# Optimization experiments

Hardware: AMD Instinct MI355X
Metric: run time of the kernel (lower is better)

## Reference

```python
import jax, jax.numpy as jnp
import numpy as np

KAPPA = 5.0
EPS_NORM = 1e-12  # torch F.normalize eps
EPS_LOG = 1e-09


def setup_inputs() -> dict:
    key = jax.random.key(0)
    student_output = jax.random.normal(key, (16384, 256), dtype=jnp.float32)
    return {"student_output": student_output}


def reference(student_output) -> jnp.ndarray:
    # L2-normalize rows (matches F.normalize: x / max(||x||, eps))
    norm = jnp.linalg.norm(student_output, axis=-1, keepdims=True)
    x_norm = student_output / jnp.maximum(norm, EPS_NORM)
    # pairwise cosine similarity [n, n]
    sim = x_norm @ x_norm.T
    kernel = jnp.exp(KAPPA * sim)
    density_estimates = kernel.sum(axis=1)  # [n]
    entropy = -jnp.mean(jnp.log(density_estimates + EPS_LOG))
    return entropy
```

## Files before the change

### kernel.cpp

```cpp
#include <hip/hip_runtime.h>


#define NROWS 16384
#define KDIM 256
#define NTILE 128
#define NT (NROWS / NTILE)
#define NSTRIP 4
#define TOTAL_BLOCKS (NT * NSTRIP)

typedef int i32x4_t __attribute__((ext_vector_type(4)));
typedef int i32x8_t __attribute__((ext_vector_type(8)));
typedef float f32x16_t __attribute__((ext_vector_type(16)));
typedef __attribute__((address_space(1))) const void global_cvoid_t;
typedef __attribute__((address_space(3))) void lds_void_t;

#if __has_builtin(__builtin_amdgcn_exp2f)
#define EXPK(x) __builtin_amdgcn_exp2f((x) * 7.2134752044448f)
#else
#define EXPK(x) __expf(5.0f * (x))
#endif

union frag8 { i32x8_t v8; i32x4_t v4[2]; };

__global__ __launch_bounds__(256)
void kde_normalize(const float* __restrict__ X, unsigned int* __restrict__ Xn8,
                   float* __restrict__ density, unsigned int* __restrict__ ticket) {
  const int wave = threadIdx.x >> 6;
  const int lane = threadIdx.x & 63;
  const int row = blockIdx.x * 4 + wave;
  const float4 v = ((const float4*)(X + (size_t)row * KDIM))[lane];
  float ss = v.x * v.x + v.y * v.y + v.z * v.z + v.w * v.w;
  ss += __shfl_xor(ss, 1);
  ss += __shfl_xor(ss, 2);
  ss += __shfl_xor(ss, 4);
  ss += __shfl_xor(ss, 8);
  ss += __shfl_xor(ss, 16);
  ss += __shfl_xor(ss, 32);
  const float scale = 1.0f / fmaxf(sqrtf(ss), 1e-12f);
  int p = 0;
  p = __builtin_amdgcn_cvt_pk_fp8_f32(v.x * scale, v.y * scale, p, false);
  p = __builtin_amdgcn_cvt_pk_fp8_f32(v.z * scale, v.w * scale, p, true);
  Xn8[(size_t)row * 64 + lane] = (unsigned int)p;
  if (threadIdx.x < 4) density[blockIdx.x * 4 + threadIdx.x] = 0.0f;
  if (blockIdx.x == 0 && threadIdx.x == 0) *ticket = 0u;
}

__global__ __launch_bounds__(256, 2)
void kde_gemm(const unsigned char* __restrict__ Xn8, float* __restrict__ density,
              unsigned int* __restrict__ ticket, float* __restrict__ out) {
  extern __shared__ char smem[];
  char* As = smem;
  char* Bs = smem + 32768;

  const int tid = threadIdx.x;
  const int wave = tid >> 6;
  const int lane = tid & 63;
  const int wr = wave >> 1;
  const int wc = wave & 1;
  const int m32 = lane & 31;
  const int h = lane >> 5;
  const int bi = blockIdx.x;
  const int s = blockIdx.y;
  const int t0 = s * 16;
  const int nt = (s == NSTRIP - 1 && bi < NT / 2) ? 17 : 16;
  const char* Xb = (const char*)Xn8;

#define STAGE(base_row, dst)                                                      \
  for (int c = wave; c < 32; c += 4) {                                            \
    const int rt = c >> 3, kb = (c >> 1) & 3, hh = c & 1;                         \
    const size_t gofs =                                                           \
        (size_t)((base_row) + rt * 32 + m32) * KDIM + kb * 64 + h * 32 + hh * 16; \
    __builtin_amdgcn_global_load_lds((global_cvoid_t*)(Xb + gofs),                \
                                     (lds_void_t*)((dst) + c * 1024), 16, 0, 0);  \
  }

  STAGE(bi * NTILE, As);
  STAGE(((bi + t0) & (NT - 1)) * NTILE, Bs);

  float rs[2][16];
#pragma unroll
  for (int i = 0; i < 2; i++)
#pragma unroll
    for (int r = 0; r < 16; r++) rs[i][r] = 0.0f;

  for (int k = 0; k < nt; ++k) {
    const int t = t0 + k;
    const int J = (bi + t) & (NT - 1);
    __syncthreads();

    f32x16_t acc[2][2];
#pragma unroll
    for (int i = 0; i < 2; i++)
#pragma unroll
      for (int j = 0; j < 2; j++) acc[i][j] = (f32x16_t)0.0f;

#pragma unroll
    for (int kb = 0; kb < 4; ++kb) {
      frag8 af[2], bf[2];
#pragma unroll
      for (int i = 0; i < 2; i++) {
        const char* pa = As + ((wr * 2 + i) * 8 + kb * 2) * 1024 + lane * 16;
        af[i].v4[0] = *(const i32x4_t*)pa;
        af[i].v4[1] = *(const i32x4_t*)(pa + 1024);
        const char* pb = Bs + ((wc * 2 + i) * 8 + kb * 2) * 1024 + lane * 16;
        bf[i].v4[0] = *(const i32x4_t*)pb;
        bf[i].v4[1] = *(const i32x4_t*)(pb + 1024);
      }
#pragma unroll
      for (int i = 0; i < 2; i++)
#pragma unroll
        for (int j = 0; j < 2; j++)
          acc[i][j] = __builtin_amdgcn_mfma_scale_f32_32x32x64_f8f6f4(
              af[i].v8, bf[j].v8, acc[i][j], 0, 0, 0, 127, 0, 127);
    }

    __syncthreads();

    if (k + 1 < nt) STAGE(((J + 1) & (NT - 1)) * NTILE, Bs);

    float cs[2] = {0.0f, 0.0f};
#pragma unroll
    for (int i = 0; i < 2; i++)
#pragma unroll
      for (int j = 0; j < 2; j++)
#pragma unroll
        for (int r = 0; r < 16; r++) {
          const float e = EXPK(acc[i][j][r]);
          rs[i][r] += e;
          cs[j] += e;
        }

    if (t != 0) {
#pragma unroll
      for (int j = 0; j < 2; j++) {
        float v = cs[j] + __shfl_xor(cs[j], 32);
        if (h == 0)
          atomicAdd(&density[J * NTILE + wc * 64 + j * 32 + m32], v);
      }
    }
  }

#pragma unroll
  for (int i = 0; i < 2; i++)
#pragma unroll
    for (int r = 0; r < 16; r++) {
      float v = rs[i][r];
      v += __shfl_xor(v, 1);
      v += __shfl_xor(v, 2);
      v += __shfl_xor(v, 4);
      v += __shfl_xor(v, 8);
      v += __shfl_xor(v, 16);
      if (m32 == 0) {
        const int row = bi * NTILE + wr * 64 + i * 32 + (r & 3) + 8 * (r >> 2) + 4 * h;
        atomicAdd(&density[row], v);
      }
    }
#undef STAGE

  __syncthreads();
  if (tid == 0) {
    __threadfence();
    ((volatile unsigned int*)smem)[0] = atomicAdd(ticket, 1u);
  }
  __syncthreads();
  if (((volatile unsigned int*)smem)[0] == TOTAL_BLOCKS - 1) {
    __threadfence();
    float ssum = 0.0f;
    for (int i = tid; i < NROWS; i += 256) {
      const float d = __hip_atomic_load(&density[i], __ATOMIC_RELAXED,
                                        __HIP_MEMORY_SCOPE_AGENT);
      ssum += logf(d + 1e-9f);
    }
    ssum += __shfl_xor(ssum, 1);
    ssum += __shfl_xor(ssum, 2);
    ssum += __shfl_xor(ssum, 4);
    ssum += __shfl_xor(ssum, 8);
    ssum += __shfl_xor(ssum, 16);
    ssum += __shfl_xor(ssum, 32);
    float* red = ((float*)smem) + 16;
    if (lane == 0) red[wave] = ssum;
    __syncthreads();
    if (tid == 0) out[0] = -(red[0] + red[1] + red[2] + red[3]) / (float)NROWS;
  }
}

extern "C" void kernel_launch(void* const* d_in, const int* in_sizes, int n_in,
                              void* d_out, int out_size, void* d_ws, size_t ws_size,
                              hipStream_t stream) {
  const float* X = (const float*)d_in[0];
  float* out = (float*)d_out;
  char* ws = (char*)d_ws;
  unsigned int* Xn8 = (unsigned int*)ws;
  float* density = (float*)(ws + (size_t)NROWS * KDIM);
  unsigned int* ticket = (unsigned int*)(density + NROWS);

  hipFuncSetAttribute((const void*)kde_gemm,
                      hipFuncAttributeMaxDynamicSharedMemorySize, 65536);

  kde_normalize<<<NROWS / 4, 256, 0, stream>>>(X, Xn8, density, ticket);
  kde_gemm<<<dim3(NT, NSTRIP), 256, 65536, stream>>>((const unsigned char*)ws,
                                                     density, ticket, out);
}
```

Before: 135.2 us.

## Double-buffer B tiles, keep A fragments in registers, fold exp scale into normalization

The B tile now uses two LDS buffers. The next tile is prefetched at the start of each iteration, so the global-to-LDS copy overlaps the MFMA and exp work, and only one barrier remains per iteration. The A tile fragments are loaded from LDS into registers once and reused across all column tiles, which removes repeated LDS reads. The exp scale factor kappa·log2(e) is split as a square root into each normalized row before fp8 quantization, so the exp becomes a bare exp2. The costs are higher register pressure and slightly different fp8 rounding of the scaled values.

```diff
diff --git a/kernel.cpp b/kernel.cpp
--- a/kernel.cpp
+++ b/kernel.cpp
@@ -8,6 +8,8 @@
 #define NSTRIP 4
 #define TOTAL_BLOCKS (NT * NSTRIP)
 
+#define SQRT_KLOG2E 2.68579577857f
+
 typedef int i32x4_t __attribute__((ext_vector_type(4)));
 typedef int i32x8_t __attribute__((ext_vector_type(8)));
 typedef float f32x16_t __attribute__((ext_vector_type(16)));
@@ -15,9 +17,9 @@
 typedef __attribute__((address_space(3))) void lds_void_t;
 
 #if __has_builtin(__builtin_amdgcn_exp2f)
-#define EXPK(x) __builtin_amdgcn_exp2f((x) * 7.2134752044448f)
+#define EXP2(x) __builtin_amdgcn_exp2f(x)
 #else
-#define EXPK(x) __expf(5.0f * (x))
+#define EXP2(x) exp2f(x)
 #endif
 
 union frag8 { i32x8_t v8; i32x4_t v4[2]; };
@@ -36,7 +38,7 @@
   ss += __shfl_xor(ss, 8);
   ss += __shfl_xor(ss, 16);
   ss += __shfl_xor(ss, 32);
-  const float scale = 1.0f / fmaxf(sqrtf(ss), 1e-12f);
+  const float scale = SQRT_KLOG2E / fmaxf(sqrtf(ss), 1e-12f);
   int p = 0;
   p = __builtin_amdgcn_cvt_pk_fp8_f32(v.x * scale, v.y * scale, p, false);
   p = __builtin_amdgcn_cvt_pk_fp8_f32(v.z * scale, v.w * scale, p, true);
@@ -49,8 +51,8 @@
 void kde_gemm(const unsigned char* __restrict__ Xn8, float* __restrict__ density,
               unsigned int* __restrict__ ticket, float* __restrict__ out) {
   extern __shared__ char smem[];
-  char* As = smem;
-  char* Bs = smem + 32768;
+  char* buf0 = smem;
+  char* buf1 = smem + 32768;
 
   const int tid = threadIdx.x;
   const int wave = tid >> 6;
@@ -74,8 +76,20 @@
                                      (lds_void_t*)((dst) + c * 1024), 16, 0, 0);  \
   }
 
-  STAGE(bi * NTILE, As);
-  STAGE(((bi + t0) & (NT - 1)) * NTILE, Bs);
+  STAGE(bi * NTILE, buf0);
+  STAGE(((bi + t0) & (NT - 1)) * NTILE, buf1);
+  __syncthreads();
+
+  frag8 areg[2][4];
+#pragma unroll
+  for (int i = 0; i < 2; i++)
+#pragma unroll
+    for (int kb = 0; kb < 4; kb++) {
+      const char* pa = buf0 + ((wr * 2 + i) * 8 + kb * 2) * 1024 + lane * 16;
+      areg[i][kb].v4[0] = *(const i32x4_t*)pa;
+      areg[i][kb].v4[1] = *(const i32x4_t*)(pa + 1024);
+    }
+  __syncthreads();
 
   float rs[2][16];
 #pragma unroll
@@ -86,7 +100,10 @@
   for (int k = 0; k < nt; ++k) {
     const int t = t0 + k;
     const int J = (bi + t) & (NT - 1);
-    __syncthreads();
+    char* rbuf = (k & 1) ? buf0 : buf1;
+    char* sbuf = (k & 1) ? buf1 : buf0;
+
+    if (k + 1 < nt) STAGE(((J + 1) & (NT - 1)) * NTILE, sbuf);
 
     f32x16_t acc[2][2];
 #pragma unroll
@@ -96,27 +113,20 @@
 
 #pragma unroll
     for (int kb = 0; kb < 4; ++kb) {
-      frag8 af[2], bf[2];
-#pragma unroll
-      for (int i = 0; i < 2; i++) {
-        const char* pa = As + ((wr * 2 + i) * 8 + kb * 2) * 1024 + lane * 16;
-        af[i].v4[0] = *(const i32x4_t*)pa;
-        af[i].v4[1] = *(const i32x4_t*)(pa + 1024);
-        const char* pb = Bs + ((wc * 2 + i) * 8 + kb * 2) * 1024 + lane * 16;
-        bf[i].v4[0] = *(const i32x4_t*)pb;
-        bf[i].v4[1] = *(const i32x4_t*)(pb + 1024);
+      frag8 bf[2];
+#pragma unroll
+      for (int j = 0; j < 2; j++) {
+        const char* pb = rbuf + ((wc * 2 + j) * 8 + kb * 2) * 1024 + lane * 16;
+        bf[j].v4[0] = *(const i32x4_t*)pb;
+        bf[j].v4[1] = *(const i32x4_t*)(pb + 1024);
       }
 #pragma unroll
       for (int i = 0; i < 2; i++)
 #pragma unroll
         for (int j = 0; j < 2; j++)
           acc[i][j] = __builtin_amdgcn_mfma_scale_f32_32x32x64_f8f6f4(
-              af[i].v8, bf[j].v8, acc[i][j], 0, 0, 0, 127, 0, 127);
-    }
-
-    __syncthreads();
-
-    if (k + 1 < nt) STAGE(((J + 1) & (NT - 1)) * NTILE, Bs);
+              areg[i][kb].v8, bf[j].v8, acc[i][j], 0, 0, 0, 127, 0, 127);
+    }
 
     float cs[2] = {0.0f, 0.0f};
 #pragma unroll
@@ -125,7 +135,7 @@
       for (int j = 0; j < 2; j++)
 #pragma unroll
         for (int r = 0; r < 16; r++) {
-          const float e = EXPK(acc[i][j][r]);
+          const float e = EXP2(acc[i][j][r]);
           rs[i][r] += e;
           cs[j] += e;
         }
@@ -138,6 +148,8 @@
           atomicAdd(&density[J * NTILE + wc * 64 + j * 32 + m32], v);
       }
     }
+
+    __syncthreads();
   }
 
 #pragma unroll
```

After: 133.7 us. Within noise of the previous version (-1.1%).
